# Optimization experiments

Measured on AMD Instinct MI355X. Metric: run time of the kernel, lower is better.

## Reference

```python
import jax, jax.numpy as jnp
import numpy as np


def _hilbert_filter(S):
    # scipy.signal.hilbert analytic-signal spectrum multiplier
    h = np.zeros(S, dtype=np.float32)
    h[0] = 1.0
    if S % 2 == 0:
        h[S // 2] = 1.0
        h[1:S // 2] = 2.0
    else:
        h[1:(S + 1) // 2] = 2.0
    return h


def setup_inputs() -> dict:
    key = jax.random.key(0)
    B, C, S = 16, 64, 2048
    x = jax.random.normal(key, (B, C, S), dtype=jnp.float32)
    return {"x": x}


def reference(x) -> jnp.ndarray:
    B, C, S = x.shape
    h = jnp.asarray(_hilbert_filter(S))
    # Analytic signal via FFT (batched over all B*C channels at once,
    # instead of recomputing hilbert() per (i,j) pair as the torch loop does)
    analytic = jnp.fft.ifft(jnp.fft.fft(x, axis=-1) * h, axis=-1)  # [B,C,S] complex
    theta = jnp.angle(analytic)                                    # [B,C,S]
    # Pairwise instantaneous phase differences: [B,C,C,S]
    d = theta[:, :, None, :] - theta[:, None, :, :]
    # angle(exp(1j*d)) wraps d to (-pi,pi]; original zeroes exact +/-pi values.
    # sign(sin(d)) == sign(wrapped d) with +/-pi (and 0) mapped to 0 -- identical math.
    pli = jnp.abs(jnp.mean(jnp.sign(jnp.sin(d)), axis=-1))         # [B,C,C]
    # diagonal: d == 0 -> sign 0 -> mean 0, matching the skipped i==j entries
    return pli.astype(jnp.float32)
```

## Files before the change

### kernel.cpp

```cpp
#include <hip/hip_runtime.h>

#define Bv 16
#define Cv 64
#define Sv 2048
#define NSEG 64
#define SSEG 32
#define ROWS 68
#define NTILE 144

__device__ __forceinline__ void bf_f(float2& u, float2& v, const float2 w) {
    const float dr = u.x - v.x, di = u.y - v.y;
    u.x += v.x; u.y += v.y;
    v.x = dr * w.x - di * w.y;
    v.y = dr * w.y + di * w.x;
}
__device__ __forceinline__ void bf_i(float2& u, float2& v, const float2 w) {
    const float vr = v.x * w.x + v.y * w.y;
    const float vi = v.y * w.x - v.x * w.y;
    v.x = u.x - vr; v.y = u.y - vi;
    u.x += vr; u.y += vi;
}
__device__ __forceinline__ float2 csq(const float2 a) {
    return make_float2(a.x * a.x - a.y * a.y, 2.0f * a.x * a.y);
}
__device__ __forceinline__ float2 cm1(const float2 a) {
    const float cq = 0.70710678118654752f;
    return make_float2(cq * (a.x + a.y), cq * (a.y - a.x));
}
__device__ __forceinline__ float2 cmi(const float2 a) {
    return make_float2(a.y, -a.x);
}
__device__ __forceinline__ int pad(int n) { return n + (n >> 3); }

__global__ __launch_bounds__(256) void hilbert_kernel(const float* __restrict__ x,
                                                      unsigned int* __restrict__ u) {
    __shared__ float2 zz[Sv + Sv / 8];
    const int t = threadIdx.x;
    const int c0 = blockIdx.x * 2;
    const float* x0 = x + (size_t)c0 * Sv;
    const float* x1 = x0 + Sv;

    const float PI = 3.14159265358979323846f;
    float2 bA4, bB4, bC2;
    sincosf(-PI * (float)t * (1.0f / 1024.0f), &bA4.y, &bA4.x);
    sincosf(-PI * (float)(t & 31) * (1.0f / 128.0f), &bB4.y, &bB4.x);
    sincosf(-PI * (float)(t & 7) * (1.0f / 16.0f), &bC2.y, &bC2.x);
    const float2 bA2 = csq(bA4), bA1 = csq(bA2);
    const float2 bB2 = csq(bB4), bB1 = csq(bB2);
    const float2 bC1 = csq(bC2);

    float2 z[8];
    #pragma unroll
    for (int k = 0; k < 8; ++k)
        z[k] = make_float2(x0[t + 256 * k], x1[t + 256 * k]);

    {
        const float2 w1 = cm1(bA4);
        bf_f(z[0], z[4], bA4);      bf_f(z[1], z[5], w1);
        bf_f(z[2], z[6], cmi(bA4)); bf_f(z[3], z[7], cmi(w1));
        const float2 wB = cmi(bA2);
        bf_f(z[0], z[2], bA2); bf_f(z[1], z[3], wB);
        bf_f(z[4], z[6], bA2); bf_f(z[5], z[7], wB);
        bf_f(z[0], z[1], bA1); bf_f(z[2], z[3], bA1);
        bf_f(z[4], z[5], bA1); bf_f(z[6], z[7], bA1);
    }
    #pragma unroll
    for (int k = 0; k < 8; ++k) zz[pad(t + 256 * k)] = z[k];
    __syncthreads();

    {
        const int r = t & 31, base = (t >> 5) * 256 + r;
        #pragma unroll
        for (int k = 0; k < 8; ++k) z[k] = zz[pad(base + 32 * k)];
        const float2 w1 = cm1(bB4);
        bf_f(z[0], z[4], bB4);      bf_f(z[1], z[5], w1);
        bf_f(z[2], z[6], cmi(bB4)); bf_f(z[3], z[7], cmi(w1));
        const float2 wB = cmi(bB2);
        bf_f(z[0], z[2], bB2); bf_f(z[1], z[3], wB);
        bf_f(z[4], z[6], bB2); bf_f(z[5], z[7], wB);
        bf_f(z[0], z[1], bB1); bf_f(z[2], z[3], bB1);
        bf_f(z[4], z[5], bB1); bf_f(z[6], z[7], bB1);
        #pragma unroll
        for (int k = 0; k < 8; ++k) zz[pad(base + 32 * k)] = z[k];
    }
    __syncthreads();

    {
        const int r = t & 7, base0 = (t >> 3) * 32 + r, base1 = base0 + 1024;
        #pragma unroll
        for (int k = 0; k < 4; ++k) {
            z[k] = zz[pad(base0 + 8 * k)];
            z[4 + k] = zz[pad(base1 + 8 * k)];
        }
        const float2 wB = cmi(bC2);
        bf_f(z[0], z[2], bC2); bf_f(z[1], z[3], wB);
        bf_f(z[4], z[6], bC2); bf_f(z[5], z[7], wB);
        bf_f(z[0], z[1], bC1); bf_f(z[2], z[3], bC1);
        bf_f(z[4], z[5], bC1); bf_f(z[6], z[7], bC1);
        #pragma unroll
        for (int k = 0; k < 4; ++k) {
            zz[pad(base0 + 8 * k)] = z[k];
            zz[pad(base1 + 8 * k)] = z[4 + k];
        }
    }
    __syncthreads();

    {
        const int base = 8 * t;
        #pragma unroll
        for (int k = 0; k < 8; ++k) z[k] = zz[pad(base + k)];
        const float cq = 0.70710678118654752f;
        const float2 W1  = make_float2(1.0f, 0.0f);
        const float2 W41 = make_float2(cq, -cq);
        const float2 W42 = make_float2(0.0f, -1.0f);
        const float2 W43 = make_float2(-cq, -cq);
        bf_f(z[0], z[4], W1);  bf_f(z[1], z[5], W41);
        bf_f(z[2], z[6], W42); bf_f(z[3], z[7], W43);
        bf_f(z[0], z[2], W1); bf_f(z[1], z[3], W42);
        bf_f(z[4], z[6], W1); bf_f(z[5], z[7], W42);
        bf_f(z[0], z[1], W1); bf_f(z[2], z[3], W1);
        bf_f(z[4], z[5], W1); bf_f(z[6], z[7], W1);
        const float inv = 1.0f / (float)Sv;
        #pragma unroll
        for (int k = 0; k < 8; ++k) {
            const int kk = (int)(__brev((unsigned)(base + k)) >> 21);
            const float m = (kk == 0 || kk == Sv / 2) ? inv : (kk < Sv / 2 ? 2.0f * inv : 0.0f);
            z[k].x *= m; z[k].y *= m;
        }
        bf_i(z[0], z[1], W1); bf_i(z[2], z[3], W1);
        bf_i(z[4], z[5], W1); bf_i(z[6], z[7], W1);
        bf_i(z[0], z[2], W1); bf_i(z[1], z[3], W42);
        bf_i(z[4], z[6], W1); bf_i(z[5], z[7], W42);
        bf_i(z[0], z[4], W1);  bf_i(z[1], z[5], W41);
        bf_i(z[2], z[6], W42); bf_i(z[3], z[7], W43);
        #pragma unroll
        for (int k = 0; k < 8; ++k) zz[pad(base + k)] = z[k];
    }
    __syncthreads();

    {
        const int r = t & 7, base0 = (t >> 3) * 32 + r, base1 = base0 + 1024;
        #pragma unroll
        for (int k = 0; k < 4; ++k) {
            z[k] = zz[pad(base0 + 8 * k)];
            z[4 + k] = zz[pad(base1 + 8 * k)];
        }
        bf_i(z[0], z[1], bC1); bf_i(z[2], z[3], bC1);
        bf_i(z[4], z[5], bC1); bf_i(z[6], z[7], bC1);
        const float2 wB = cmi(bC2);
        bf_i(z[0], z[2], bC2); bf_i(z[1], z[3], wB);
        bf_i(z[4], z[6], bC2); bf_i(z[5], z[7], wB);
        #pragma unroll
        for (int k = 0; k < 4; ++k) {
            zz[pad(base0 + 8 * k)] = z[k];
            zz[pad(base1 + 8 * k)] = z[4 + k];
        }
    }
    __syncthreads();

    {
        const int r = t & 31, base = (t >> 5) * 256 + r;
        #pragma unroll
        for (int k = 0; k < 8; ++k) z[k] = zz[pad(base + 32 * k)];
        bf_i(z[0], z[1], bB1); bf_i(z[2], z[3], bB1);
        bf_i(z[4], z[5], bB1); bf_i(z[6], z[7], bB1);
        const float2 wB = cmi(bB2);
        bf_i(z[0], z[2], bB2); bf_i(z[1], z[3], wB);
        bf_i(z[4], z[6], bB2); bf_i(z[5], z[7], wB);
        const float2 w1 = cm1(bB4);
        bf_i(z[0], z[4], bB4);      bf_i(z[1], z[5], w1);
        bf_i(z[2], z[6], cmi(bB4)); bf_i(z[3], z[7], cmi(w1));
        #pragma unroll
        for (int k = 0; k < 8; ++k) zz[pad(base + 32 * k)] = z[k];
    }
    __syncthreads();

    {
        #pragma unroll
        for (int k = 0; k < 8; ++k) z[k] = zz[pad(t + 256 * k)];
        bf_i(z[0], z[1], bA1); bf_i(z[2], z[3], bA1);
        bf_i(z[4], z[5], bA1); bf_i(z[6], z[7], bA1);
        const float2 wB = cmi(bA2);
        bf_i(z[0], z[2], bA2); bf_i(z[1], z[3], wB);
        bf_i(z[4], z[6], bA2); bf_i(z[5], z[7], wB);
        const float2 w1 = cm1(bA4);
        bf_i(z[0], z[4], bA4);      bf_i(z[1], z[5], w1);
        bf_i(z[2], z[6], cmi(bA4)); bf_i(z[3], z[7], cmi(w1));
        unsigned int* u0 = u + (size_t)c0 * Sv;
        unsigned int* u1 = u0 + Sv;
        const float SC = 683565275.576f;
        #pragma unroll
        for (int k = 0; k < 8; ++k) {
            const int n = t + 256 * k;
            const float xa = x0[n], xb = x1[n];
            const float ha = z[k].y - xb;
            const float hb = xa - z[k].x;
            u0[n] = (unsigned int)__float2int_rz(atan2f(ha, xa) * SC);
            u1[n] = (unsigned int)__float2int_rz(atan2f(hb, xb) * SC);
        }
    }
}

__global__ __launch_bounds__(256) void pli_count_kernel(const unsigned int* __restrict__ u,
                                                        unsigned int* __restrict__ part) {
    __shared__ __align__(16) unsigned int uL[SSEG * ROWS];
    const int blk = blockIdx.x;
    const int seg = blk & (NSEG - 1);
    const int b = blk >> 6;
    const int t = threadIdx.x;
    const unsigned int* ub = u + (size_t)b * Cv * Sv + seg * SSEG;

    for (int e = t; e < Cv * SSEG; e += 256) {
        const int ch = e >> 5;
        const int s = e & (SSEG - 1);
        uL[s * ROWS + ch] = ub[(size_t)ch * Sv + s];
    }
    __syncthreads();

    if (t < NTILE) {
        const int qi = t & 15;
        const int dq = t >> 4;
        const int i0 = qi * 4;
        const int j0 = ((qi + dq) & 15) * 4;
        int neg[4][4] = {};

        #pragma unroll 4
        for (int s = 0; s < SSEG; ++s) {
            const uint4 ui = *(const uint4*)&uL[s * ROWS + i0];
            const uint4 uj = *(const uint4*)&uL[s * ROWS + j0];
            const unsigned int uia[4] = {ui.x, ui.y, ui.z, ui.w};
            const unsigned int uja[4] = {uj.x, uj.y, uj.z, uj.w};
            #pragma unroll
            for (int a = 0; a < 4; ++a) {
                #pragma unroll
                for (int c = 0; c < 4; ++c) {
                    neg[a][c] += (int)((uia[a] - uja[c]) >> 31);
                }
            }
        }

        unsigned int* Pb = part + ((size_t)blk * NTILE + t) * 4;
        unsigned int pk[4];
        #pragma unroll
        for (int a = 0; a < 4; ++a)
            pk[a] = (unsigned)neg[a][0] | ((unsigned)neg[a][1] << 8)
                  | ((unsigned)neg[a][2] << 16) | ((unsigned)neg[a][3] << 24);
        *(uint4*)Pb = make_uint4(pk[0], pk[1], pk[2], pk[3]);
    }
}

__global__ __launch_bounds__(256) void finalize_kernel(const unsigned char* __restrict__ part,
                                                       float* __restrict__ out) {
    const int idx = blockIdx.x * 256 + threadIdx.x;
    const int b = idx >> 12;
    const int ij = idx & 4095;
    const int i = ij >> 6, j = ij & 63;
    const int qi = i >> 2, a = i & 3;
    const int qj = j >> 2, c = j & 3;
    const int g = (qj - qi) & 15;
    int byteoff;
    if (g <= 8) byteoff = (g * 16 + qi) * 16 + a * 4 + c;
    else        byteoff = ((16 - g) * 16 + qj) * 16 + c * 4 + a;
    const unsigned char* p = part + (size_t)b * NSEG * (NTILE * 16) + byteoff;
    int negsum = 0;
    #pragma unroll 8
    for (int s = 0; s < NSEG; ++s)
        negsum += (int)p[s * (NTILE * 16)];
    out[idx] = (i == j) ? 0.0f
                        : fabsf((float)Sv - 2.0f * (float)negsum) * (1.0f / (float)Sv);
}

extern "C" void kernel_launch(void* const* d_in, const int* in_sizes, int n_in,
                              void* d_out, int out_size, void* d_ws, size_t ws_size,
                              hipStream_t stream) {
    const float* x = (const float*)d_in[0];
    unsigned int* u = (unsigned int*)d_ws;
    unsigned int* part = (unsigned int*)((char*)d_ws + (size_t)Bv * Cv * Sv * sizeof(unsigned int));
    float* out = (float*)d_out;

    hipLaunchKernelGGL(hilbert_kernel, dim3(Bv * Cv / 2), dim3(256), 0, stream, x, u);
    hipLaunchKernelGGL(pli_count_kernel, dim3(Bv * NSEG), dim3(256), 0, stream, u, part);
    hipLaunchKernelGGL(finalize_kernel, dim3(Bv * Cv * Cv / 256), dim3(256), 0, stream,
                       (const unsigned char*)part, out);
}
```

Baseline: 81.66 us.

## Fuse Hilbert, pairwise count and finalize into one cooperative kernel

Merges the three kernels into a single cooperative launch of 512 blocks, separated by grid-wide syncs, and reuses one shared-memory buffer for both the FFT workspace and the transposed phase tile. The segment split is changed to 32 segments of 64 samples so that the count phase maps one segment per block. The input samples stay in registers for the final phase computation instead of being reloaded. This removes inter-kernel launch gaps and a global re-read. In exchange it pays for two grid barriers, needs all blocks resident at once (enforced with a 2-blocks-per-CU launch bound), and leaves half the blocks idle during finalize.

```diff
diff --git a/kernel.cpp b/kernel.cpp
--- a/kernel.cpp
+++ b/kernel.cpp
@@ -1,10 +1,13 @@
 #include <hip/hip_runtime.h>
+#include <hip/hip_cooperative_groups.h>
+
+namespace cg = cooperative_groups;
 
 #define Bv 16
 #define Cv 64
 #define Sv 2048
-#define NSEG 64
-#define SSEG 32
+#define NSEG 32
+#define SSEG 64
 #define ROWS 68
 #define NTILE 144
 
@@ -32,242 +35,258 @@
 }
 __device__ __forceinline__ int pad(int n) { return n + (n >> 3); }
 
-__global__ __launch_bounds__(256) void hilbert_kernel(const float* __restrict__ x,
-                                                      unsigned int* __restrict__ u) {
-    __shared__ float2 zz[Sv + Sv / 8];
+__global__ __launch_bounds__(256, 2) void pli_fused(const float* __restrict__ x,
+                                                    unsigned int* __restrict__ u,
+                                                    unsigned int* __restrict__ part,
+                                                    float* __restrict__ out) {
+    __shared__ __align__(16) unsigned char shraw[(Sv + Sv / 8) * sizeof(float2)];
+    float2* const zz = (float2*)shraw;
+    unsigned int* const uL = (unsigned int*)shraw;
     const int t = threadIdx.x;
-    const int c0 = blockIdx.x * 2;
-    const float* x0 = x + (size_t)c0 * Sv;
-    const float* x1 = x0 + Sv;
-
-    const float PI = 3.14159265358979323846f;
-    float2 bA4, bB4, bC2;
-    sincosf(-PI * (float)t * (1.0f / 1024.0f), &bA4.y, &bA4.x);
-    sincosf(-PI * (float)(t & 31) * (1.0f / 128.0f), &bB4.y, &bB4.x);
-    sincosf(-PI * (float)(t & 7) * (1.0f / 16.0f), &bC2.y, &bC2.x);
-    const float2 bA2 = csq(bA4), bA1 = csq(bA2);
-    const float2 bB2 = csq(bB4), bB1 = csq(bB2);
-    const float2 bC1 = csq(bC2);
-
-    float2 z[8];
-    #pragma unroll
-    for (int k = 0; k < 8; ++k)
-        z[k] = make_float2(x0[t + 256 * k], x1[t + 256 * k]);
+    cg::grid_group grid = cg::this_grid();
 
     {
-        const float2 w1 = cm1(bA4);
-        bf_f(z[0], z[4], bA4);      bf_f(z[1], z[5], w1);
-        bf_f(z[2], z[6], cmi(bA4)); bf_f(z[3], z[7], cmi(w1));
-        const float2 wB = cmi(bA2);
-        bf_f(z[0], z[2], bA2); bf_f(z[1], z[3], wB);
-        bf_f(z[4], z[6], bA2); bf_f(z[5], z[7], wB);
-        bf_f(z[0], z[1], bA1); bf_f(z[2], z[3], bA1);
-        bf_f(z[4], z[5], bA1); bf_f(z[6], z[7], bA1);
-    }
-    #pragma unroll
-    for (int k = 0; k < 8; ++k) zz[pad(t + 256 * k)] = z[k];
-    __syncthreads();
-
-    {
-        const int r = t & 31, base = (t >> 5) * 256 + r;
-        #pragma unroll
-        for (int k = 0; k < 8; ++k) z[k] = zz[pad(base + 32 * k)];
-        const float2 w1 = cm1(bB4);
-        bf_f(z[0], z[4], bB4);      bf_f(z[1], z[5], w1);
-        bf_f(z[2], z[6], cmi(bB4)); bf_f(z[3], z[7], cmi(w1));
-        const float2 wB = cmi(bB2);
-        bf_f(z[0], z[2], bB2); bf_f(z[1], z[3], wB);
-        bf_f(z[4], z[6], bB2); bf_f(z[5], z[7], wB);
-        bf_f(z[0], z[1], bB1); bf_f(z[2], z[3], bB1);
-        bf_f(z[4], z[5], bB1); bf_f(z[6], z[7], bB1);
-        #pragma unroll
-        for (int k = 0; k < 8; ++k) zz[pad(base + 32 * k)] = z[k];
-    }
-    __syncthreads();
-
-    {
-        const int r = t & 7, base0 = (t >> 3) * 32 + r, base1 = base0 + 1024;
-        #pragma unroll
-        for (int k = 0; k < 4; ++k) {
-            z[k] = zz[pad(base0 + 8 * k)];
-            z[4 + k] = zz[pad(base1 + 8 * k)];
-        }
-        const float2 wB = cmi(bC2);
-        bf_f(z[0], z[2], bC2); bf_f(z[1], z[3], wB);
-        bf_f(z[4], z[6], bC2); bf_f(z[5], z[7], wB);
-        bf_f(z[0], z[1], bC1); bf_f(z[2], z[3], bC1);
-        bf_f(z[4], z[5], bC1); bf_f(z[6], z[7], bC1);
-        #pragma unroll
-        for (int k = 0; k < 4; ++k) {
-            zz[pad(base0 + 8 * k)] = z[k];
-            zz[pad(base1 + 8 * k)] = z[4 + k];
-        }
-    }
-    __syncthreads();
-
-    {
-        const int base = 8 * t;
-        #pragma unroll
-        for (int k = 0; k < 8; ++k) z[k] = zz[pad(base + k)];
-        const float cq = 0.70710678118654752f;
-        const float2 W1  = make_float2(1.0f, 0.0f);
-        const float2 W41 = make_float2(cq, -cq);
-        const float2 W42 = make_float2(0.0f, -1.0f);
-        const float2 W43 = make_float2(-cq, -cq);
-        bf_f(z[0], z[4], W1);  bf_f(z[1], z[5], W41);
-        bf_f(z[2], z[6], W42); bf_f(z[3], z[7], W43);
-        bf_f(z[0], z[2], W1); bf_f(z[1], z[3], W42);
-        bf_f(z[4], z[6], W1); bf_f(z[5], z[7], W42);
-        bf_f(z[0], z[1], W1); bf_f(z[2], z[3], W1);
-        bf_f(z[4], z[5], W1); bf_f(z[6], z[7], W1);
-        const float inv = 1.0f / (float)Sv;
+        const int c0 = blockIdx.x * 2;
+        const float* x0 = x + (size_t)c0 * Sv;
+        const float* x1 = x0 + Sv;
+
+        const float PI = 3.14159265358979323846f;
+        float2 bA4, bB4, bC2;
+        sincosf(-PI * (float)t * (1.0f / 1024.0f), &bA4.y, &bA4.x);
+        sincosf(-PI * (float)(t & 31) * (1.0f / 128.0f), &bB4.y, &bB4.x);
+        sincosf(-PI * (float)(t & 7) * (1.0f / 16.0f), &bC2.y, &bC2.x);
+        const float2 bA2 = csq(bA4), bA1 = csq(bA2);
+        const float2 bB2 = csq(bB4), bB1 = csq(bB2);
+        const float2 bC1 = csq(bC2);
+
+        float xa[8], xb[8];
+        float2 z[8];
         #pragma unroll
         for (int k = 0; k < 8; ++k) {
-            const int kk = (int)(__brev((unsigned)(base + k)) >> 21);
-            const float m = (kk == 0 || kk == Sv / 2) ? inv : (kk < Sv / 2 ? 2.0f * inv : 0.0f);
-            z[k].x *= m; z[k].y *= m;
-        }
-        bf_i(z[0], z[1], W1); bf_i(z[2], z[3], W1);
-        bf_i(z[4], z[5], W1); bf_i(z[6], z[7], W1);
-        bf_i(z[0], z[2], W1); bf_i(z[1], z[3], W42);
-        bf_i(z[4], z[6], W1); bf_i(z[5], z[7], W42);
-        bf_i(z[0], z[4], W1);  bf_i(z[1], z[5], W41);
-        bf_i(z[2], z[6], W42); bf_i(z[3], z[7], W43);
+            xa[k] = x0[t + 256 * k];
+            xb[k] = x1[t + 256 * k];
+            z[k] = make_float2(xa[k], xb[k]);
+        }
+
+        {
+            const float2 w1 = cm1(bA4);
+            bf_f(z[0], z[4], bA4);      bf_f(z[1], z[5], w1);
+            bf_f(z[2], z[6], cmi(bA4)); bf_f(z[3], z[7], cmi(w1));
+            const float2 wB = cmi(bA2);
+            bf_f(z[0], z[2], bA2); bf_f(z[1], z[3], wB);
+            bf_f(z[4], z[6], bA2); bf_f(z[5], z[7], wB);
+            bf_f(z[0], z[1], bA1); bf_f(z[2], z[3], bA1);
+            bf_f(z[4], z[5], bA1); bf_f(z[6], z[7], bA1);
+        }
         #pragma unroll
-        for (int k = 0; k < 8; ++k) zz[pad(base + k)] = z[k];
+        for (int k = 0; k < 8; ++k) zz[pad(t + 256 * k)] = z[k];
+        __syncthreads();
+
+        {
+            const int r = t & 31, base = (t >> 5) * 256 + r;
+            #pragma unroll
+            for (int k = 0; k < 8; ++k) z[k] = zz[pad(base + 32 * k)];
+            const float2 w1 = cm1(bB4);
+            bf_f(z[0], z[4], bB4);      bf_f(z[1], z[5], w1);
+            bf_f(z[2], z[6], cmi(bB4)); bf_f(z[3], z[7], cmi(w1));
+            const float2 wB = cmi(bB2);
+            bf_f(z[0], z[2], bB2); bf_f(z[1], z[3], wB);
+            bf_f(z[4], z[6], bB2); bf_f(z[5], z[7], wB);
+            bf_f(z[0], z[1], bB1); bf_f(z[2], z[3], bB1);
+            bf_f(z[4], z[5], bB1); bf_f(z[6], z[7], bB1);
+            #pragma unroll
+            for (int k = 0; k < 8; ++k) zz[pad(base + 32 * k)] = z[k];
+        }
+        __syncthreads();
+
+        {
+            const int r = t & 7, base0 = (t >> 3) * 32 + r, base1 = base0 + 1024;
+            #pragma unroll
+            for (int k = 0; k < 4; ++k) {
+                z[k] = zz[pad(base0 + 8 * k)];
+                z[4 + k] = zz[pad(base1 + 8 * k)];
+            }
+            const float2 wB = cmi(bC2);
+            bf_f(z[0], z[2], bC2); bf_f(z[1], z[3], wB);
+            bf_f(z[4], z[6], bC2); bf_f(z[5], z[7], wB);
+            bf_f(z[0], z[1], bC1); bf_f(z[2], z[3], bC1);
+            bf_f(z[4], z[5], bC1); bf_f(z[6], z[7], bC1);
+            #pragma unroll
+            for (int k = 0; k < 4; ++k) {
+                zz[pad(base0 + 8 * k)] = z[k];
+                zz[pad(base1 + 8 * k)] = z[4 + k];
+            }
+        }
+        __syncthreads();
+
+        {
+            const int base = 8 * t;
+            #pragma unroll
+            for (int k = 0; k < 8; ++k) z[k] = zz[pad(base + k)];
+            const float cq = 0.70710678118654752f;
+            const float2 W1  = make_float2(1.0f, 0.0f);
+            const float2 W41 = make_float2(cq, -cq);
+            const float2 W42 = make_float2(0.0f, -1.0f);
+            const float2 W43 = make_float2(-cq, -cq);
+            bf_f(z[0], z[4], W1);  bf_f(z[1], z[5], W41);
+            bf_f(z[2], z[6], W42); bf_f(z[3], z[7], W43);
+            bf_f(z[0], z[2], W1); bf_f(z[1], z[3], W42);
+            bf_f(z[4], z[6], W1); bf_f(z[5], z[7], W42);
+            bf_f(z[0], z[1], W1); bf_f(z[2], z[3], W1);
+            bf_f(z[4], z[5], W1); bf_f(z[6], z[7], W1);
+            const float inv = 1.0f / (float)Sv;
+            #pragma unroll
+            for (int k = 0; k < 8; ++k) {
+                const int kk = (int)(__brev((unsigned)(base + k)) >> 21);
+                const float m = (kk == 0 || kk == Sv / 2) ? inv : (kk < Sv / 2 ? 2.0f * inv : 0.0f);
+                z[k].x *= m; z[k].y *= m;
+            }
+            bf_i(z[0], z[1], W1); bf_i(z[2], z[3], W1);
+            bf_i(z[4], z[5], W1); bf_i(z[6], z[7], W1);
+            bf_i(z[0], z[2], W1); bf_i(z[1], z[3], W42);
+            bf_i(z[4], z[6], W1); bf_i(z[5], z[7], W42);
+            bf_i(z[0], z[4], W1);  bf_i(z[1], z[5], W41);
+            bf_i(z[2], z[6], W42); bf_i(z[3], z[7], W43);
+            #pragma unroll
+            for (int k = 0; k < 8; ++k) zz[pad(base + k)] = z[k];
+        }
+        __syncthreads();
+
+        {
+            const int r = t & 7, base0 = (t >> 3) * 32 + r, base1 = base0 + 1024;
+            #pragma unroll
+            for (int k = 0; k < 4; ++k) {
+                z[k] = zz[pad(base0 + 8 * k)];
+                z[4 + k] = zz[pad(base1 + 8 * k)];
+            }
+            bf_i(z[0], z[1], bC1); bf_i(z[2], z[3], bC1);
+            bf_i(z[4], z[5], bC1); bf_i(z[6], z[7], bC1);
+            const float2 wB = cmi(bC2);
+            bf_i(z[0], z[2], bC2); bf_i(z[1], z[3], wB);
+            bf_i(z[4], z[6], bC2); bf_i(z[5], z[7], wB);
+            #pragma unroll
+            for (int k = 0; k < 4; ++k) {
+                zz[pad(base0 + 8 * k)] = z[k];
+                zz[pad(base1 + 8 * k)] = z[4 + k];
+            }
+        }
+        __syncthreads();
+
+        {
+            const int r = t & 31, base = (t >> 5) * 256 + r;
+            #pragma unroll
+            for (int k = 0; k < 8; ++k) z[k] = zz[pad(base + 32 * k)];
+            bf_i(z[0], z[1], bB1); bf_i(z[2], z[3], bB1);
+            bf_i(z[4], z[5], bB1); bf_i(z[6], z[7], bB1);
+            const float2 wB = cmi(bB2);
+            bf_i(z[0], z[2], bB2); bf_i(z[1], z[3], wB);
+            bf_i(z[4], z[6], bB2); bf_i(z[5], z[7], wB);
+            const float2 w1 = cm1(bB4);
+            bf_i(z[0], z[4], bB4);      bf_i(z[1], z[5], w1);
+            bf_i(z[2], z[6], cmi(bB4)); bf_i(z[3], z[7], cmi(w1));
+            #pragma unroll
+            for (int k = 0; k < 8; ++k) zz[pad(base + 32 * k)] = z[k];
+        }
+        __syncthreads();
+
+        {
+            #pragma unroll
+            for (int k = 0; k < 8; ++k) z[k] = zz[pad(t + 256 * k)];
+            bf_i(z[0], z[1], bA1); bf_i(z[2], z[3], bA1);
+            bf_i(z[4], z[5], bA1); bf_i(z[6], z[7], bA1);
+            const float2 wB = cmi(bA2);
+            bf_i(z[0], z[2], bA2); bf_i(z[1], z[3], wB);
+            bf_i(z[4], z[6], bA2); bf_i(z[5], z[7], wB);
+            const float2 w1 = cm1(bA4);
+            bf_i(z[0], z[4], bA4);      bf_i(z[1], z[5], w1);
+            bf_i(z[2], z[6], cmi(bA4)); bf_i(z[3], z[7], cmi(w1));
+            unsigned int* u0 = u + (size_t)c0 * Sv;
+            unsigned int* u1 = u0 + Sv;
+            const float SC = 683565275.576f;
+            #pragma unroll
+            for (int k = 0; k < 8; ++k) {
+                const int n = t + 256 * k;
+                const float ha = z[k].y - xb[k];
+                const float hb = xa[k] - z[k].x;
+                u0[n] = (unsigned int)__float2int_rz(atan2f(ha, xa[k]) * SC);
+                u1[n] = (unsigned int)__float2int_rz(atan2f(hb, xb[k]) * SC);
+            }
+        }
     }
-    __syncthreads();
+
+    grid.sync();
 
     {
-        const int r = t & 7, base0 = (t >> 3) * 32 + r, base1 = base0 + 1024;
+        const int blk = blockIdx.x;
+        const int g = blk & (NSEG - 1);
+        const int b = blk >> 5;
+        const unsigned int* ub = u + (size_t)b * Cv * Sv + g * SSEG;
+
         #pragma unroll
-        for (int k = 0; k < 4; ++k) {
-            z[k] = zz[pad(base0 + 8 * k)];
-            z[4 + k] = zz[pad(base1 + 8 * k)];
-        }
-        bf_i(z[0], z[1], bC1); bf_i(z[2], z[3], bC1);
-        bf_i(z[4], z[5], bC1); bf_i(z[6], z[7], bC1);
-        const float2 wB = cmi(bC2);
-        bf_i(z[0], z[2], bC2); bf_i(z[1], z[3], wB);
-        bf_i(z[4], z[6], bC2); bf_i(z[5], z[7], wB);
-        #pragma unroll
-        for (int k = 0; k < 4; ++k) {
-            zz[pad(base0 + 8 * k)] = z[k];
-            zz[pad(base1 + 8 * k)] = z[4 + k];
+        for (int it = 0; it < 16; ++it) {
+            const int e = t + 256 * it;
+            const int ch = e >> 6;
+            const int s = e & (SSEG - 1);
+            uL[s * ROWS + ch] = ub[(size_t)ch * Sv + s];
+        }
+        __syncthreads();
+
+        if (t < NTILE) {
+            const int qi = t & 15;
+            const int dq = t >> 4;
+            const int i0 = qi * 4;
+            const int j0 = ((qi + dq) & 15) * 4;
+            int neg[4][4] = {};
+
+            #pragma unroll 4
+            for (int s = 0; s < SSEG; ++s) {
+                const uint4 ui = *(const uint4*)&uL[s * ROWS + i0];
+                const uint4 uj = *(const uint4*)&uL[s * ROWS + j0];
+                const unsigned int uia[4] = {ui.x, ui.y, ui.z, ui.w};
+                const unsigned int uja[4] = {uj.x, uj.y, uj.z, uj.w};
+                #pragma unroll
+                for (int a = 0; a < 4; ++a) {
+                    #pragma unroll
+                    for (int c = 0; c < 4; ++c) {
+                        neg[a][c] += (int)((uia[a] - uja[c]) >> 31);
+                    }
+                }
+            }
+
+            unsigned int* Pb = part + ((size_t)blk * NTILE + t) * 4;
+            unsigned int pk[4];
+            #pragma unroll
+            for (int a = 0; a < 4; ++a)
+                pk[a] = (unsigned)neg[a][0] | ((unsigned)neg[a][1] << 8)
+                      | ((unsigned)neg[a][2] << 16) | ((unsigned)neg[a][3] << 24);
+            *(uint4*)Pb = make_uint4(pk[0], pk[1], pk[2], pk[3]);
         }
     }
-    __syncthreads();
+
+    grid.sync();
 
     {
-        const int r = t & 31, base = (t >> 5) * 256 + r;
-        #pragma unroll
-        for (int k = 0; k < 8; ++k) z[k] = zz[pad(base + 32 * k)];
-        bf_i(z[0], z[1], bB1); bf_i(z[2], z[3], bB1);
-        bf_i(z[4], z[5], bB1); bf_i(z[6], z[7], bB1);
-        const float2 wB = cmi(bB2);
-        bf_i(z[0], z[2], bB2); bf_i(z[1], z[3], wB);
-        bf_i(z[4], z[6], bB2); bf_i(z[5], z[7], wB);
-        const float2 w1 = cm1(bB4);
-        bf_i(z[0], z[4], bB4);      bf_i(z[1], z[5], w1);
-        bf_i(z[2], z[6], cmi(bB4)); bf_i(z[3], z[7], cmi(w1));
-        #pragma unroll
-        for (int k = 0; k < 8; ++k) zz[pad(base + 32 * k)] = z[k];
+        const int idx = blockIdx.x * 256 + t;
+        if (idx < Bv * Cv * Cv) {
+            const unsigned char* pc = (const unsigned char*)part;
+            const int b = idx >> 12;
+            const int ij = idx & 4095;
+            const int i = ij >> 6, j = ij & 63;
+            const int qi = i >> 2, a = i & 3;
+            const int qj = j >> 2, c = j & 3;
+            const int gg = (qj - qi) & 15;
+            int byteoff;
+            if (gg <= 8) byteoff = (gg * 16 + qi) * 16 + a * 4 + c;
+            else         byteoff = ((16 - gg) * 16 + qj) * 16 + c * 4 + a;
+            const unsigned char* p = pc + (size_t)b * NSEG * (NTILE * 16) + byteoff;
+            int negsum = 0;
+            #pragma unroll 8
+            for (int s = 0; s < NSEG; ++s)
+                negsum += (int)p[s * (NTILE * 16)];
+            out[idx] = (i == j) ? 0.0f
+                                : fabsf((float)Sv - 2.0f * (float)negsum) * (1.0f / (float)Sv);
+        }
     }
-    __syncthreads();
-
-    {
-        #pragma unroll
-        for (int k = 0; k < 8; ++k) z[k] = zz[pad(t + 256 * k)];
-        bf_i(z[0], z[1], bA1); bf_i(z[2], z[3], bA1);
-        bf_i(z[4], z[5], bA1); bf_i(z[6], z[7], bA1);
-        const float2 wB = cmi(bA2);
-        bf_i(z[0], z[2], bA2); bf_i(z[1], z[3], wB);
-        bf_i(z[4], z[6], bA2); bf_i(z[5], z[7], wB);
-        const float2 w1 = cm1(bA4);
-        bf_i(z[0], z[4], bA4);      bf_i(z[1], z[5], w1);
-        bf_i(z[2], z[6], cmi(bA4)); bf_i(z[3], z[7], cmi(w1));
-        unsigned int* u0 = u + (size_t)c0 * Sv;
-        unsigned int* u1 = u0 + Sv;
-        const float SC = 683565275.576f;
-        #pragma unroll
-        for (int k = 0; k < 8; ++k) {
-            const int n = t + 256 * k;
-            const float xa = x0[n], xb = x1[n];
-            const float ha = z[k].y - xb;
-            const float hb = xa - z[k].x;
-            u0[n] = (unsigned int)__float2int_rz(atan2f(ha, xa) * SC);
-            u1[n] = (unsigned int)__float2int_rz(atan2f(hb, xb) * SC);
-        }
-    }
-}
-
-__global__ __launch_bounds__(256) void pli_count_kernel(const unsigned int* __restrict__ u,
-                                                        unsigned int* __restrict__ part) {
-    __shared__ __align__(16) unsigned int uL[SSEG * ROWS];
-    const int blk = blockIdx.x;
-    const int seg = blk & (NSEG - 1);
-    const int b = blk >> 6;
-    const int t = threadIdx.x;
-    const unsigned int* ub = u + (size_t)b * Cv * Sv + seg * SSEG;
-
-    for (int e = t; e < Cv * SSEG; e += 256) {
-        const int ch = e >> 5;
-        const int s = e & (SSEG - 1);
-        uL[s * ROWS + ch] = ub[(size_t)ch * Sv + s];
-    }
-    __syncthreads();
-
-    if (t < NTILE) {
-        const int qi = t & 15;
-        const int dq = t >> 4;
-        const int i0 = qi * 4;
-        const int j0 = ((qi + dq) & 15) * 4;
-        int neg[4][4] = {};
-
-        #pragma unroll 4
-        for (int s = 0; s < SSEG; ++s) {
-            const uint4 ui = *(const uint4*)&uL[s * ROWS + i0];
-            const uint4 uj = *(const uint4*)&uL[s * ROWS + j0];
-            const unsigned int uia[4] = {ui.x, ui.y, ui.z, ui.w};
-            const unsigned int uja[4] = {uj.x, uj.y, uj.z, uj.w};
-            #pragma unroll
-            for (int a = 0; a < 4; ++a) {
-                #pragma unroll
-                for (int c = 0; c < 4; ++c) {
-                    neg[a][c] += (int)((uia[a] - uja[c]) >> 31);
-                }
-            }
-        }
-
-        unsigned int* Pb = part + ((size_t)blk * NTILE + t) * 4;
-        unsigned int pk[4];
-        #pragma unroll
-        for (int a = 0; a < 4; ++a)
-            pk[a] = (unsigned)neg[a][0] | ((unsigned)neg[a][1] << 8)
-                  | ((unsigned)neg[a][2] << 16) | ((unsigned)neg[a][3] << 24);
-        *(uint4*)Pb = make_uint4(pk[0], pk[1], pk[2], pk[3]);
-    }
-}
-
-__global__ __launch_bounds__(256) void finalize_kernel(const unsigned char* __restrict__ part,
-                                                       float* __restrict__ out) {
-    const int idx = blockIdx.x * 256 + threadIdx.x;
-    const int b = idx >> 12;
-    const int ij = idx & 4095;
-    const int i = ij >> 6, j = ij & 63;
-    const int qi = i >> 2, a = i & 3;
-    const int qj = j >> 2, c = j & 3;
-    const int g = (qj - qi) & 15;
-    int byteoff;
-    if (g <= 8) byteoff = (g * 16 + qi) * 16 + a * 4 + c;
-    else        byteoff = ((16 - g) * 16 + qj) * 16 + c * 4 + a;
-    const unsigned char* p = part + (size_t)b * NSEG * (NTILE * 16) + byteoff;
-    int negsum = 0;
-    #pragma unroll 8
-    for (int s = 0; s < NSEG; ++s)
-        negsum += (int)p[s * (NTILE * 16)];
-    out[idx] = (i == j) ? 0.0f
-                        : fabsf((float)Sv - 2.0f * (float)negsum) * (1.0f / (float)Sv);
 }
 
 extern "C" void kernel_launch(void* const* d_in, const int* in_sizes, int n_in,
@@ -278,8 +297,7 @@
     unsigned int* part = (unsigned int*)((char*)d_ws + (size_t)Bv * Cv * Sv * sizeof(unsigned int));
     float* out = (float*)d_out;
 
-    hipLaunchKernelGGL(hilbert_kernel, dim3(Bv * Cv / 2), dim3(256), 0, stream, x, u);
-    hipLaunchKernelGGL(pli_count_kernel, dim3(Bv * NSEG), dim3(256), 0, stream, u, part);
-    hipLaunchKernelGGL(finalize_kernel, dim3(Bv * Cv * Cv / 256), dim3(256), 0, stream,
-                       (const unsigned char*)part, out);
-}
+    void* args[] = { (void*)&x, (void*)&u, (void*)&part, (void*)&out };
+    hipLaunchCooperativeKernel((void*)pli_fused, dim3(Bv * Cv / 2), dim3(256),
+                               args, 0, stream);
+}
```

Result: slower. 179.2 us (+119.5%).
